# Kernel tuning notes

Measured on AMD Instinct MI355X. Metric: run time of the kernel, lower is better.

Reference implementation:

```python
import jax, jax.numpy as jnp
import numpy as np

EPS = 1e-9

def setup_inputs() -> dict:
    key = jax.random.key(0)
    ks = jax.random.split(key, 6)
    B, S, D, F, E, K = 2, 2048, 1024, 4096, 8, 2
    hidden = jax.random.normal(ks[0], (B, S, D), dtype=jnp.float32)
    expert_indices = jax.random.randint(ks[1], (B, S, K), 0, E, dtype=jnp.int32)
    expert_weights = jax.random.uniform(ks[2], (B, S, K), dtype=jnp.float32)
    # normalize like a real top-k router would
    expert_weights = expert_weights / jnp.sum(expert_weights, axis=-1, keepdims=True)
    router_logits = jax.random.normal(ks[3], (B, S, E), dtype=jnp.float32)
    w1 = jax.random.normal(ks[4], (E, D, F), dtype=jnp.float32) * (1.0 / np.sqrt(D))
    b1 = jnp.zeros((E, F), dtype=jnp.float32)
    w2 = jax.random.normal(ks[5], (E, F, D), dtype=jnp.float32) * (1.0 / np.sqrt(F))
    b2 = jnp.zeros((E, D), dtype=jnp.float32)
    return {"hidden": hidden, "expert_indices": expert_indices,
            "expert_weights": expert_weights, "router_logits": router_logits,
            "w1": w1, "b1": b1, "w2": w2, "b2": b2}

def reference(hidden, expert_indices, expert_weights, router_logits, w1, b1, w2, b2):
    # All-expert dense compute (faithful to torch.stack([expert(hidden) ...], dim=-2))
    # hidden: [B,S,D]; w1: [E,D,F]; w2: [E,F,D]
    h1 = jnp.einsum('bsd,edf->bsef', hidden, w1) + b1            # [B,S,E,F]
    h1 = jax.nn.gelu(h1)
    expert_outputs = jnp.einsum('bsef,efd->bsed', h1, w2) + b2   # [B,S,E,D]
    # gather selected experts along expert axis (torch.gather dim=-2)
    idx = expert_indices[..., None]                              # [B,S,K,1]
    selected = jnp.take_along_axis(expert_outputs, idx, axis=-2) # [B,S,K,D]
    mixed = jnp.sum(selected * expert_weights[..., None], axis=-2)  # [B,S,D]
    # observation stats
    route_probs = jax.nn.softmax(router_logits, axis=-1)
    log_p = jnp.log(jnp.clip(route_probs, EPS, None))
    route_entropy = jnp.mean(jnp.sum(-route_probs * log_p, axis=-1))
    top2 = jax.lax.top_k(route_probs, 2)[0]
    winner_margin = jnp.mean(top2[..., 0] - top2[..., -1])
    return (mixed, route_entropy, winner_margin)
```

## Files before the change

kernel.cpp:

```cpp
#include <hip/hip_runtime.h>
#include <stddef.h>
#include <stdint.h>

#define BDIM 2
#define SDIM 2048
#define DDIM 1024
#define FDIM 4096
#define ENUM 8
#define KSEL 2
#define TTOK (BDIM * SDIM)
#define PPAIR (TTOK * KSEL)
#define VOUT ((size_t)TTOK * DDIM)

typedef float f32x4 __attribute__((ext_vector_type(4)));
typedef short bf16x8 __attribute__((ext_vector_type(8)));
typedef unsigned short u16x8 __attribute__((ext_vector_type(8)));
typedef unsigned short u16x4 __attribute__((ext_vector_type(4)));

#define WAITV(N) asm volatile("s_waitcnt vmcnt(" #N ")" ::: "memory")
#define BARX() asm volatile("s_barrier" ::: "memory")

__device__ __forceinline__ unsigned short f2bf(float f) {
  unsigned int u = __float_as_uint(f);
  u += 0x7fffu + ((u >> 16) & 1u);
  return (unsigned short)(u >> 16);
}

__device__ __forceinline__ float gelu_tanh(float x) {
  float u = 0.7978845608028654f * (x + 0.044715f * x * x * x);
  float e = __expf(2.0f * u);
  float t = 1.0f - 2.0f / (e + 1.0f);
  return 0.5f * x * (1.0f + t);
}

__device__ __forceinline__ void gload16(const void* g, void* l) {
  __builtin_amdgcn_global_load_lds(
      (const __attribute__((address_space(1))) unsigned int*)g,
      (__attribute__((address_space(3))) unsigned int*)l, 16, 0, 0);
}

__global__ __launch_bounds__(256) void statsA_kernel(const float* __restrict__ lg,
                                                     float* __restrict__ pst) {
  __shared__ float se[256], sm[256];
  const int r = blockIdx.x * 256 + threadIdx.x;
  float v[ENUM];
  float mx = -1e30f;
#pragma unroll
  for (int i = 0; i < ENUM; ++i) { v[i] = lg[r * ENUM + i]; mx = fmaxf(mx, v[i]); }
  float s = 0.f;
#pragma unroll
  for (int i = 0; i < ENUM; ++i) { v[i] = __expf(v[i] - mx); s += v[i]; }
  float inv = 1.f / s;
  float p1 = -1.f, p2 = -1.f, e_ = 0.f;
#pragma unroll
  for (int i = 0; i < ENUM; ++i) {
    float p = v[i] * inv;
    e_ -= p * logf(fmaxf(p, 1e-9f));
    if (p > p1) { p2 = p1; p1 = p; } else if (p > p2) { p2 = p; }
  }
  se[threadIdx.x] = e_; sm[threadIdx.x] = p1 - p2;
  __syncthreads();
  for (int st = 128; st > 0; st >>= 1) {
    if (threadIdx.x < (unsigned)st) { se[threadIdx.x] += se[threadIdx.x + st]; sm[threadIdx.x] += sm[threadIdx.x + st]; }
    __syncthreads();
  }
  if (threadIdx.x == 0) { pst[blockIdx.x * 2] = se[0]; pst[blockIdx.x * 2 + 1] = sm[0]; }
}

__global__ void statsB_kernel(const float* __restrict__ pst, float* __restrict__ out) {
  if (threadIdx.x == 0) {
    float a = 0.f, b = 0.f;
    for (int i = 0; i < 16; ++i) { a += pst[2 * i]; b += pst[2 * i + 1]; }
    out[VOUT]     = a / (float)TTOK;
    out[VOUT + 1] = b / (float)TTOK;
  }
}

__global__ __launch_bounds__(256) void routing_kernel(const int* __restrict__ eidx,
                                                      int* __restrict__ g_cnt,
                                                      int* __restrict__ g_off,
                                                      int* __restrict__ pairTok,
                                                      int* __restrict__ inv,
                                                      int* __restrict__ b256E,
                                                      int* __restrict__ b256M,
                                                      int* __restrict__ b128E,
                                                      int* __restrict__ b128M,
                                                      int* __restrict__ nT) {
  __shared__ int sc[ENUM], so[ENUM], scur[ENUM];
  const int tid = threadIdx.x;
  if (tid < ENUM) sc[tid] = 0;
  __syncthreads();
  for (int p = tid; p < PPAIR; p += 256) atomicAdd(&sc[eidx[p]], 1);
  __syncthreads();
  if (tid == 0) {
    int o = 0, n256 = 0, n128 = 0;
    for (int e = 0; e < ENUM; ++e) {
      so[e] = o;
      const int cnt = sc[e];
      const int nf = cnt >> 8;
      const int rem = cnt - (nf << 8);
      for (int i = 0; i < nf; ++i) { b256E[n256] = e; b256M[n256] = i << 8; ++n256; }
      const int np = (rem + 127) >> 7;
      for (int j = 0; j < np; ++j) { b128E[n128] = e; b128M[n128] = (nf << 8) + (j << 7); ++n128; }
      o += cnt;
    }
    nT[0] = n256; nT[1] = n128;
  }
  __syncthreads();
  if (tid < ENUM) { scur[tid] = so[tid]; g_cnt[tid] = sc[tid]; g_off[tid] = so[tid]; }
  __syncthreads();
  for (int p = tid; p < PPAIR; p += 256) {
    int e = eidx[p];
    int pos = atomicAdd(&scur[e], 1);
    pairTok[pos] = p >> 1;
    inv[p] = pos;
  }
}

__global__ __launch_bounds__(256) void cvt_hidden_kernel(const float* __restrict__ in,
                                                         unsigned short* __restrict__ outp) {
  const int i = blockIdx.x * 256 + threadIdx.x;
  f32x4 a = ((const f32x4*)in)[(size_t)i * 2];
  f32x4 b = ((const f32x4*)in)[(size_t)i * 2 + 1];
  u16x8 o;
  o[0] = f2bf(a[0]); o[1] = f2bf(a[1]); o[2] = f2bf(a[2]); o[3] = f2bf(a[3]);
  o[4] = f2bf(b[0]); o[5] = f2bf(b[1]); o[6] = f2bf(b[2]); o[7] = f2bf(b[3]);
  ((u16x8*)outp)[i] = o;
}

__global__ __launch_bounds__(256) void transpose_cvt_kernel(const float* __restrict__ in,
                                                            unsigned short* __restrict__ outp,
                                                            int R, int C) {
  __shared__ float tile[32][33];
  const size_t base = (size_t)blockIdx.z * (size_t)R * (size_t)C;
  const float* ip = in + base;
  unsigned short* op = outp + base;
  const int r0 = blockIdx.y * 32, c0 = blockIdx.x * 32;
  const int i = threadIdx.x >> 3;
  const int j4 = (threadIdx.x & 7) << 2;
  f32x4 v = *(const f32x4*)(ip + (size_t)(r0 + i) * C + c0 + j4);
  tile[i][j4 + 0] = v[0]; tile[i][j4 + 1] = v[1]; tile[i][j4 + 2] = v[2]; tile[i][j4 + 3] = v[3];
  __syncthreads();
  u16x4 o;
  o[0] = f2bf(tile[j4 + 0][i]); o[1] = f2bf(tile[j4 + 1][i]);
  o[2] = f2bf(tile[j4 + 2][i]); o[3] = f2bf(tile[j4 + 3][i]);
  *(u16x4*)(op + (size_t)(c0 + i) * R + r0 + j4) = o;
}

__global__ __launch_bounds__(512, 2) void gemm1_kernel(const unsigned short* __restrict__ hB,
                                                       const unsigned short* __restrict__ w1T,
                                                       const float* __restrict__ b1,
                                                       const int* __restrict__ g_off,
                                                       const int* __restrict__ pairTok,
                                                       const int* __restrict__ b256E,
                                                       const int* __restrict__ b256M,
                                                       const int* __restrict__ nT,
                                                       unsigned short* __restrict__ h1) {
  const int flat = blockIdx.x + 32 * blockIdx.y;
  const int w = (flat & 7) * 64 + (flat >> 3);
  const int mI = w & 31;
  const int nB = w >> 5;
  if (mI >= nT[0]) return;
  const int e = b256E[mI];
  const int m0 = b256M[mI];
  const int off_e = g_off[e];
  const int n0 = nB << 8;

  __shared__ __align__(16) unsigned short Ah[2][2][256 * 32];
  __shared__ __align__(16) unsigned short Bh[2][2][256 * 32];

  const int tid = threadIdx.x;
  const int lane = tid & 63;
  const int wm = (tid >> 6) >> 2;
  const int wn = (tid >> 6) & 3;

  const unsigned short* gArow[2];
  const unsigned short* gBrow[2];
  int ldsOff[2];
#pragma unroll
  for (int c = 0; c < 2; ++c) {
    const int idx = c * 512 + tid;
    const int row = idx >> 2;
    const int g = (idx & 3) ^ ((row >> 1) & 3);
    ldsOff[c] = idx * 16;
    const int tok = pairTok[off_e + m0 + row];
    gArow[c] = hB + (size_t)tok * DDIM + g * 8;
    gBrow[c] = w1T + ((size_t)e * FDIM + (n0 + row)) * DDIM + g * 8;
  }

#define G1_STAGE_A(bufv, ksv, kofs) do { \
  gload16(gArow[0] + (kofs), (char*)(&Ah[(bufv)][(ksv)][0]) + ldsOff[0]); \
  gload16(gArow[1] + (kofs), (char*)(&Ah[(bufv)][(ksv)][0]) + ldsOff[1]); } while (0)
#define G1_STAGE_B(bufv, ksv, kofs) do { \
  gload16(gBrow[0] + (kofs), (char*)(&Bh[(bufv)][(ksv)][0]) + ldsOff[0]); \
  gload16(gBrow[1] + (kofs), (char*)(&Bh[(bufv)][(ksv)][0]) + ldsOff[1]); } while (0)

  const int kh = lane >> 4;
  const int l15 = lane & 15;
  int aoff[8], boff[4];
#pragma unroll
  for (int i = 0; i < 8; ++i) {
    const int r = wm * 128 + i * 16 + l15;
    aoff[i] = r * 64 + ((kh ^ ((r >> 1) & 3)) << 4);
  }
#pragma unroll
  for (int i = 0; i < 4; ++i) {
    const int r = wn * 64 + i * 16 + l15;
    boff[i] = r * 64 + ((kh ^ ((r >> 1) & 3)) << 4);
  }

  f32x4 acc[8][4];
#pragma unroll
  for (int i = 0; i < 8; ++i)
#pragma unroll
    for (int j = 0; j < 4; ++j) acc[i][j] = (f32x4){0.f, 0.f, 0.f, 0.f};

  const int KT = DDIM / 64;
  G1_STAGE_A(0, 0, 0);  G1_STAGE_B(0, 0, 0);
  G1_STAGE_A(0, 1, 32); G1_STAGE_B(0, 1, 32);
  G1_STAGE_A(1, 0, 64); G1_STAGE_B(1, 0, 64);
  G1_STAGE_A(1, 1, 96);
  WAITV(6);
  BARX();

  for (int t = 0; t < KT; ++t) {
    const int buf = t & 1;
    const int bufn = buf ^ 1;
    const int ko1 = (t + 1) * 64;
    const int ko2 = (t + 2) * 64;
    bf16x8 af[4], bv[4];
#pragma unroll
    for (int ks = 0; ks < 2; ++ks) {
#pragma unroll
      for (int i = 0; i < 4; ++i) bv[i] = *(const bf16x8*)((const char*)(&Bh[buf][ks][0]) + boff[i]);
#pragma unroll
      for (int i = 0; i < 4; ++i) af[i] = *(const bf16x8*)((const char*)(&Ah[buf][ks][0]) + aoff[i]);
      __builtin_amdgcn_s_setprio(1);
#pragma unroll
      for (int mi = 0; mi < 4; ++mi)
#pragma unroll
        for (int ni = 0; ni < 4; ++ni)
          acc[mi][ni] = __builtin_amdgcn_mfma_f32_16x16x32_bf16(af[mi], bv[ni], acc[mi][ni], 0, 0, 0);
      __builtin_amdgcn_s_setprio(0);
      if (ks == 0) { if (t + 1 < KT) G1_STAGE_B(bufn, 1, ko1 + 32); }
      else         { if (t + 2 < KT) G1_STAGE_B(buf, 0, ko2); }
      BARX();
#pragma unroll
      for (int i = 0; i < 4; ++i) af[i] = *(const bf16x8*)((const char*)(&Ah[buf][ks][0]) + aoff[4 + i]);
      __builtin_amdgcn_s_setprio(1);
#pragma unroll
      for (int mi = 0; mi < 4; ++mi)
#pragma unroll
        for (int ni = 0; ni < 4; ++ni)
          acc[4 + mi][ni] = __builtin_amdgcn_mfma_f32_16x16x32_bf16(af[mi], bv[ni], acc[4 + mi][ni], 0, 0, 0);
      __builtin_amdgcn_s_setprio(0);
      if (ks == 0) { if (t + 2 < KT) G1_STAGE_A(buf, 0, ko2); }
      else {
        if (t + 2 < KT) G1_STAGE_A(buf, 1, ko2 + 32);
        if (t < KT - 2)      { WAITV(6); }
        else if (t == KT - 2){ WAITV(0); }
      }
      BARX();
    }
  }
#undef G1_STAGE_A
#undef G1_STAGE_B

  float bias[4];
#pragma unroll
  for (int ni = 0; ni < 4; ++ni)
    bias[ni] = b1[e * FDIM + n0 + wn * 64 + ni * 16 + l15];
#pragma unroll
  for (int mi = 0; mi < 8; ++mi) {
#pragma unroll
    for (int j = 0; j < 4; ++j) {
      const int row = wm * 128 + mi * 16 + kh * 4 + j;
      unsigned short* dst = h1 + (size_t)(off_e + m0 + row) * FDIM + n0 + wn * 64;
#pragma unroll
      for (int ni = 0; ni < 4; ++ni)
        dst[ni * 16 + l15] = f2bf(gelu_tanh(acc[mi][ni][j] + bias[ni]));
    }
  }
}

__global__ __launch_bounds__(512, 2) void gemm1p_kernel(const unsigned short* __restrict__ hB,
                                                        const unsigned short* __restrict__ w1T,
                                                        const float* __restrict__ b1,
                                                        const int* __restrict__ g_cnt,
                                                        const int* __restrict__ g_off,
                                                        const int* __restrict__ pairTok,
                                                        const int* __restrict__ b128E,
                                                        const int* __restrict__ b128M,
                                                        const int* __restrict__ nT,
                                                        unsigned short* __restrict__ h1) {
  const int flat = blockIdx.x + 16 * blockIdx.y;
  const int w = (flat & 7) * 32 + (flat >> 3);
  const int mI = w & 15;
  const int nB = w >> 4;
  if (mI >= nT[1]) return;
  const int e = b128E[mI];
  const int m0 = b128M[mI];
  const int off_e = g_off[e];
  const int rows_e = min(128, g_cnt[e] - m0);
  const int n0 = nB << 8;

  __shared__ __align__(16) unsigned short As[2][128 * 64];
  __shared__ __align__(16) unsigned short Bs[2][256 * 64];

  const int tid = threadIdx.x;
  const int lane = tid & 63;
  const int wm = (tid >> 6) >> 2;
  const int wn = (tid >> 6) & 3;

  const unsigned short* gA[2];
  const unsigned short* gB[4];
  int ldsA[2], ldsB[4];
#pragma unroll
  for (int c = 0; c < 2; ++c) {
    const int p = (c * 512 + tid) * 16;
    const int row = p >> 7;
    const int g = ((p >> 4) & 7) ^ (row & 7);
    ldsA[c] = p;
    const int tok = pairTok[off_e + m0 + min(row, rows_e - 1)];
    gA[c] = hB + (size_t)tok * DDIM + (g << 3);
  }
#pragma unroll
  for (int c = 0; c < 4; ++c) {
    const int p = (c * 512 + tid) * 16;
    const int row = p >> 7;
    const int g = ((p >> 4) & 7) ^ (row & 7);
    ldsB[c] = p;
    gB[c] = w1T + ((size_t)e * FDIM + (n0 + row)) * DDIM + (g << 3);
  }

  const int kh = lane >> 4;
  const int l15 = lane & 15;
  int aoff[4][2], boff[4][2];
#pragma unroll
  for (int i = 0; i < 4; ++i) {
    const int ar = wm * 64 + i * 16 + l15;
#pragma unroll
    for (int ks = 0; ks < 2; ++ks)
      aoff[i][ks] = ar * 128 + ((((ks << 2) | kh) ^ (ar & 7)) << 4);
    const int br = wn * 64 + i * 16 + l15;
#pragma unroll
    for (int ks = 0; ks < 2; ++ks)
      boff[i][ks] = br * 128 + ((((ks << 2) | kh) ^ (br & 7)) << 4);
  }

  f32x4 acc[4][4];
#pragma unroll
  for (int i = 0; i < 4; ++i)
#pragma unroll
    for (int j = 0; j < 4; ++j) acc[i][j] = (f32x4){0.f, 0.f, 0.f, 0.f};

#pragma unroll
  for (int c = 0; c < 2; ++c) gload16(gA[c], (char*)As[0] + ldsA[c]);
#pragma unroll
  for (int c = 0; c < 4; ++c) gload16(gB[c], (char*)Bs[0] + ldsB[c]);
  WAITV(0);
  BARX();

  int cur = 0;
  const int KT = DDIM / 64;
  for (int kt = 0; kt < KT; ++kt) {
    if (kt + 1 < KT) {
#pragma unroll
      for (int c = 0; c < 2; ++c) gload16(gA[c] + (size_t)(kt + 1) * 64, (char*)As[cur ^ 1] + ldsA[c]);
#pragma unroll
      for (int c = 0; c < 4; ++c) gload16(gB[c] + (size_t)(kt + 1) * 64, (char*)Bs[cur ^ 1] + ldsB[c]);
    }
#pragma unroll
    for (int ks = 0; ks < 2; ++ks) {
      bf16x8 af[4], bv[4];
#pragma unroll
      for (int i = 0; i < 4; ++i) af[i] = *(const bf16x8*)((const char*)As[cur] + aoff[i][ks]);
#pragma unroll
      for (int i = 0; i < 4; ++i) bv[i] = *(const bf16x8*)((const char*)Bs[cur] + boff[i][ks]);
      __builtin_amdgcn_s_setprio(1);
#pragma unroll
      for (int mi = 0; mi < 4; ++mi)
#pragma unroll
        for (int ni = 0; ni < 4; ++ni)
          acc[mi][ni] = __builtin_amdgcn_mfma_f32_16x16x32_bf16(af[mi], bv[ni], acc[mi][ni], 0, 0, 0);
      __builtin_amdgcn_s_setprio(0);
    }
    WAITV(0);
    BARX();
    cur ^= 1;
  }

  float bias[4];
#pragma unroll
  for (int ni = 0; ni < 4; ++ni)
    bias[ni] = b1[e * FDIM + n0 + wn * 64 + ni * 16 + l15];
#pragma unroll
  for (int mi = 0; mi < 4; ++mi) {
#pragma unroll
    for (int j = 0; j < 4; ++j) {
      const int row = wm * 64 + mi * 16 + kh * 4 + j;
      if (row < rows_e) {
        unsigned short* dst = h1 + (size_t)(off_e + m0 + row) * FDIM + n0 + wn * 64;
#pragma unroll
        for (int ni = 0; ni < 4; ++ni)
          dst[ni * 16 + l15] = f2bf(gelu_tanh(acc[mi][ni][j] + bias[ni]));
      }
    }
  }
}

__global__ __launch_bounds__(512, 2) void gemm2_kernel(const unsigned short* __restrict__ h1,
                                                       const unsigned short* __restrict__ w2T,
                                                       const float* __restrict__ b2,
                                                       const int* __restrict__ g_off,
                                                       const int* __restrict__ b256E,
                                                       const int* __restrict__ b256M,
                                                       const int* __restrict__ nT,
                                                       float* __restrict__ h2p) {
  const int flat = blockIdx.x + 32 * blockIdx.y;
  const int w = (flat & 7) * 16 + (flat >> 3);
  const int mI = w & 31;
  const int nB = w >> 5;
  if (mI >= nT[0]) return;
  const int s = blockIdx.z;
  const int e = b256E[mI];
  const int m0 = b256M[mI];
  const int off_e = g_off[e];
  const int n0 = nB << 8;
  const int kbase = s * (FDIM / 2);

  __shared__ __align__(16) unsigned short Ah[2][2][256 * 32];
  __shared__ __align__(16) unsigned short Bh[2][2][256 * 32];

  const int tid = threadIdx.x;
  const int lane = tid & 63;
  const int wm = (tid >> 6) >> 2;
  const int wn = (tid >> 6) & 3;

  const unsigned short* gArow[2];
  const unsigned short* gBrow[2];
  int ldsOff[2];
#pragma unroll
  for (int c = 0; c < 2; ++c) {
    const int idx = c * 512 + tid;
    const int row = idx >> 2;
    const int g = (idx & 3) ^ ((row >> 1) & 3);
    ldsOff[c] = idx * 16;
    gArow[c] = h1 + (size_t)(off_e + m0 + row) * FDIM + kbase + g * 8;
    gBrow[c] = w2T + ((size_t)e * DDIM + (n0 + row)) * FDIM + kbase + g * 8;
  }

#define G2_STAGE_A(bufv, ksv, kofs) do { \
  gload16(gArow[0] + (kofs), (char*)(&Ah[(bufv)][(ksv)][0]) + ldsOff[0]); \
  gload16(gArow[1] + (kofs), (char*)(&Ah[(bufv)][(ksv)][0]) + ldsOff[1]); } while (0)
#define G2_STAGE_B(bufv, ksv, kofs) do { \
  gload16(gBrow[0] + (kofs), (char*)(&Bh[(bufv)][(ksv)][0]) + ldsOff[0]); \
  gload16(gBrow[1] + (kofs), (char*)(&Bh[(bufv)][(ksv)][0]) + ldsOff[1]); } while (0)

  const int kh = lane >> 4;
  const int l15 = lane & 15;
  int aoff[8], boff[4];
#pragma unroll
  for (int i = 0; i < 8; ++i) {
    const int r = wm * 128 + i * 16 + l15;
    aoff[i] = r * 64 + ((kh ^ ((r >> 1) & 3)) << 4);
  }
#pragma unroll
  for (int i = 0; i < 4; ++i) {
    const int r = wn * 64 + i * 16 + l15;
    boff[i] = r * 64 + ((kh ^ ((r >> 1) & 3)) << 4);
  }

  f32x4 acc[8][4];
#pragma unroll
  for (int i = 0; i < 8; ++i)
#pragma unroll
    for (int j = 0; j < 4; ++j) acc[i][j] = (f32x4){0.f, 0.f, 0.f, 0.f};

  const int KT = (FDIM / 2) / 64;
  G2_STAGE_A(0, 0, 0);  G2_STAGE_B(0, 0, 0);
  G2_STAGE_A(0, 1, 32); G2_STAGE_B(0, 1, 32);
  G2_STAGE_A(1, 0, 64); G2_STAGE_B(1, 0, 64);
  G2_STAGE_A(1, 1, 96);
  WAITV(6);
  BARX();

  for (int t = 0; t < KT; ++t) {
    const int buf = t & 1;
    const int bufn = buf ^ 1;
    const int ko1 = (t + 1) * 64;
    const int ko2 = (t + 2) * 64;
    bf16x8 af[4], bv[4];
#pragma unroll
    for (int ks = 0; ks < 2; ++ks) {
#pragma unroll
      for (int i = 0; i < 4; ++i) bv[i] = *(const bf16x8*)((const char*)(&Bh[buf][ks][0]) + boff[i]);
#pragma unroll
      for (int i = 0; i < 4; ++i) af[i] = *(const bf16x8*)((const char*)(&Ah[buf][ks][0]) + aoff[i]);
      __builtin_amdgcn_s_setprio(1);
#pragma unroll
      for (int mi = 0; mi < 4; ++mi)
#pragma unroll
        for (int ni = 0; ni < 4; ++ni)
          acc[mi][ni] = __builtin_amdgcn_mfma_f32_16x16x32_bf16(af[mi], bv[ni], acc[mi][ni], 0, 0, 0);
      __builtin_amdgcn_s_setprio(0);
      if (ks == 0) { if (t + 1 < KT) G2_STAGE_B(bufn, 1, ko1 + 32); }
      else         { if (t + 2 < KT) G2_STAGE_B(buf, 0, ko2); }
      BARX();
#pragma unroll
      for (int i = 0; i < 4; ++i) af[i] = *(const bf16x8*)((const char*)(&Ah[buf][ks][0]) + aoff[4 + i]);
      __builtin_amdgcn_s_setprio(1);
#pragma unroll
      for (int mi = 0; mi < 4; ++mi)
#pragma unroll
        for (int ni = 0; ni < 4; ++ni)
          acc[4 + mi][ni] = __builtin_amdgcn_mfma_f32_16x16x32_bf16(af[mi], bv[ni], acc[4 + mi][ni], 0, 0, 0);
      __builtin_amdgcn_s_setprio(0);
      if (ks == 0) { if (t + 2 < KT) G2_STAGE_A(buf, 0, ko2); }
      else {
        if (t + 2 < KT) G2_STAGE_A(buf, 1, ko2 + 32);
        if (t < KT - 2)      { WAITV(6); }
        else if (t == KT - 2){ WAITV(0); }
      }
      BARX();
    }
  }
#undef G2_STAGE_A
#undef G2_STAGE_B

  float* outBase = h2p + (size_t)s * PPAIR * DDIM;
#pragma unroll
  for (int mi = 0; mi < 8; ++mi) {
#pragma unroll
    for (int j = 0; j < 4; ++j) {
      const int row = wm * 128 + mi * 16 + kh * 4 + j;
      float* dp = outBase + (size_t)(off_e + m0 + row) * DDIM;
#pragma unroll
      for (int ni = 0; ni < 4; ++ni) {
        const int col = n0 + wn * 64 + ni * 16 + l15;
        float v = acc[mi][ni][j];
        if (s == 0) v += b2[e * DDIM + col];
        dp[col] = v;
      }
    }
  }
}

__global__ __launch_bounds__(512, 2) void gemm2p_kernel(const unsigned short* __restrict__ h1,
                                                        const unsigned short* __restrict__ w2T,
                                                        const float* __restrict__ b2,
                                                        const int* __restrict__ g_cnt,
                                                        const int* __restrict__ g_off,
                                                        const int* __restrict__ b128E,
                                                        const int* __restrict__ b128M,
                                                        const int* __restrict__ nT,
                                                        float* __restrict__ h2p) {
  const int flat = blockIdx.x + 16 * blockIdx.y;
  const int w = (flat & 7) * 8 + (flat >> 3);
  const int mI = w & 15;
  const int nB = w >> 4;
  if (mI >= nT[1]) return;
  const int s = blockIdx.z;
  const int e = b128E[mI];
  const int m0 = b128M[mI];
  const int off_e = g_off[e];
  const int rows_e = min(128, g_cnt[e] - m0);
  const int n0 = nB << 8;
  const int kbase = s * (FDIM / 2);

  __shared__ __align__(16) unsigned short As[2][128 * 64];
  __shared__ __align__(16) unsigned short Bs[2][256 * 64];

  const int tid = threadIdx.x;
  const int lane = tid & 63;
  const int wm = (tid >> 6) >> 2;
  const int wn = (tid >> 6) & 3;

  const unsigned short* gA[2];
  const unsigned short* gB[4];
  int ldsA[2], ldsB[4];
#pragma unroll
  for (int c = 0; c < 2; ++c) {
    const int p = (c * 512 + tid) * 16;
    const int row = p >> 7;
    const int g = ((p >> 4) & 7) ^ (row & 7);
    ldsA[c] = p;
    gA[c] = h1 + (size_t)(off_e + m0 + min(row, rows_e - 1)) * FDIM + kbase + (g << 3);
  }
#pragma unroll
  for (int c = 0; c < 4; ++c) {
    const int p = (c * 512 + tid) * 16;
    const int row = p >> 7;
    const int g = ((p >> 4) & 7) ^ (row & 7);
    ldsB[c] = p;
    gB[c] = w2T + ((size_t)e * DDIM + (n0 + row)) * FDIM + kbase + (g << 3);
  }

  const int kh = lane >> 4;
  const int l15 = lane & 15;
  int aoff[4][2], boff[4][2];
#pragma unroll
  for (int i = 0; i < 4; ++i) {
    const int ar = wm * 64 + i * 16 + l15;
    const int br = wn * 64 + i * 16 + l15;
#pragma unroll
    for (int ks = 0; ks < 2; ++ks) {
      aoff[i][ks] = ar * 128 + ((((ks << 2) | kh) ^ (ar & 7)) << 4);
      boff[i][ks] = br * 128 + ((((ks << 2) | kh) ^ (br & 7)) << 4);
    }
  }

  f32x4 acc[4][4];
#pragma unroll
  for (int i = 0; i < 4; ++i)
#pragma unroll
    for (int j = 0; j < 4; ++j) acc[i][j] = (f32x4){0.f, 0.f, 0.f, 0.f};

#pragma unroll
  for (int c = 0; c < 2; ++c) gload16(gA[c], (char*)As[0] + ldsA[c]);
#pragma unroll
  for (int c = 0; c < 4; ++c) gload16(gB[c], (char*)Bs[0] + ldsB[c]);
  WAITV(0);
  BARX();

  int cur = 0;
  const int KT = (FDIM / 2) / 64;
  for (int kt = 0; kt < KT; ++kt) {
    if (kt + 1 < KT) {
#pragma unroll
      for (int c = 0; c < 2; ++c) gload16(gA[c] + (size_t)(kt + 1) * 64, (char*)As[cur ^ 1] + ldsA[c]);
#pragma unroll
      for (int c = 0; c < 4; ++c) gload16(gB[c] + (size_t)(kt + 1) * 64, (char*)Bs[cur ^ 1] + ldsB[c]);
    }
#pragma unroll
    for (int ks = 0; ks < 2; ++ks) {
      bf16x8 af[4], bv[4];
#pragma unroll
      for (int i = 0; i < 4; ++i) af[i] = *(const bf16x8*)((const char*)As[cur] + aoff[i][ks]);
#pragma unroll
      for (int i = 0; i < 4; ++i) bv[i] = *(const bf16x8*)((const char*)Bs[cur] + boff[i][ks]);
      __builtin_amdgcn_s_setprio(1);
#pragma unroll
      for (int mi = 0; mi < 4; ++mi)
#pragma unroll
        for (int ni = 0; ni < 4; ++ni)
          acc[mi][ni] = __builtin_amdgcn_mfma_f32_16x16x32_bf16(af[mi], bv[ni], acc[mi][ni], 0, 0, 0);
      __builtin_amdgcn_s_setprio(0);
    }
    WAITV(0);
    BARX();
    cur ^= 1;
  }

  float* outBase = h2p + (size_t)s * PPAIR * DDIM;
#pragma unroll
  for (int mi = 0; mi < 4; ++mi) {
#pragma unroll
    for (int j = 0; j < 4; ++j) {
      const int row = wm * 64 + mi * 16 + kh * 4 + j;
      if (row < rows_e) {
        float* dp = outBase + (size_t)(off_e + m0 + row) * DDIM;
#pragma unroll
        for (int ni = 0; ni < 4; ++ni) {
          const int col = n0 + wn * 64 + ni * 16 + l15;
          float v = acc[mi][ni][j];
          if (s == 0) v += b2[e * DDIM + col];
          dp[col] = v;
        }
      }
    }
  }
}

__global__ __launch_bounds__(256) void combine_kernel(const float* __restrict__ h2p,
                                                      const float* __restrict__ ew,
                                                      const int* __restrict__ inv,
                                                      float* __restrict__ out) {
  const int i = blockIdx.x * 256 + threadIdx.x;
  const int t = i >> 8;
  const int c = i & 255;
  const int q0 = inv[t * 2], q1 = inv[t * 2 + 1];
  const float wa = ew[t * 2], wb = ew[t * 2 + 1];
  const f32x4* p0 = (const f32x4*)h2p;
  const f32x4* p1 = (const f32x4*)(h2p + (size_t)PPAIR * DDIM);
  f32x4 r = (p0[(size_t)q0 * 256 + c] + p1[(size_t)q0 * 256 + c]) * wa
          + (p0[(size_t)q1 * 256 + c] + p1[(size_t)q1 * 256 + c]) * wb;
  ((f32x4*)out)[i] = r;
}

extern "C" void kernel_launch(void* const* d_in, const int* in_sizes, int n_in,
                              void* d_out, int out_size, void* d_ws, size_t ws_size,
                              hipStream_t stream) {
  (void)in_sizes; (void)n_in; (void)out_size; (void)ws_size;
  const float* hidden = (const float*)d_in[0];
  const int*   eidx   = (const int*)d_in[1];
  const float* ew     = (const float*)d_in[2];
  const float* rlog   = (const float*)d_in[3];
  const float* w1     = (const float*)d_in[4];
  const float* b1     = (const float*)d_in[5];
  const float* w2     = (const float*)d_in[6];
  const float* b2     = (const float*)d_in[7];
  float* out = (float*)d_out;

  char* wsb = (char*)d_ws;
  const size_t SZ_W = (size_t)ENUM * DDIM * FDIM * 2;
  unsigned short* w1T = (unsigned short*)(wsb);
  unsigned short* w2T = (unsigned short*)(wsb + SZ_W);
  unsigned short* hB  = (unsigned short*)(wsb + 2 * SZ_W);
  unsigned short* h1  = (unsigned short*)(wsb + 2 * SZ_W + (size_t)TTOK * DDIM * 2);
  int* g_cnt   = (int*)(wsb + 2 * SZ_W + (size_t)TTOK * DDIM * 2 + (size_t)PPAIR * FDIM * 2);
  int* g_off   = g_cnt + 8;
  int* pairTok = g_off + 8;
  int* inv     = pairTok + PPAIR;
  int* b256E   = inv + PPAIR;
  int* b256M   = b256E + 32;
  int* b128E   = b256M + 32;
  int* b128M   = b128E + 16;
  int* nT      = b128M + 16;
  float* pstats = (float*)(nT + 2);
  float* h2p = (float*)wsb;

  statsA_kernel<<<16, 256, 0, stream>>>(rlog, pstats);
  statsB_kernel<<<1, 64, 0, stream>>>(pstats, out);
  routing_kernel<<<1, 256, 0, stream>>>(eidx, g_cnt, g_off, pairTok, inv, b256E, b256M, b128E, b128M, nT);
  cvt_hidden_kernel<<<(TTOK * DDIM / 8 + 255) / 256, 256, 0, stream>>>(hidden, hB);
  transpose_cvt_kernel<<<dim3(FDIM / 32, DDIM / 32, ENUM), 256, 0, stream>>>(w1, w1T, DDIM, FDIM);
  transpose_cvt_kernel<<<dim3(DDIM / 32, FDIM / 32, ENUM), 256, 0, stream>>>(w2, w2T, FDIM, DDIM);
  gemm1_kernel<<<dim3(32, 16), 512, 0, stream>>>(hB, w1T, b1, g_off, pairTok, b256E, b256M, nT, h1);
  gemm1p_kernel<<<dim3(16, 16), 512, 0, stream>>>(hB, w1T, b1, g_cnt, g_off, pairTok, b128E, b128M, nT, h1);
  gemm2_kernel<<<dim3(32, 4, 2), 512, 0, stream>>>(h1, w2T, b2, g_off, b256E, b256M, nT, h2p);
  gemm2p_kernel<<<dim3(16, 4, 2), 512, 0, stream>>>(h1, w2T, b2, g_cnt, g_off, b128E, b128M, nT, h2p);
  combine_kernel<<<(TTOK * DDIM / 4) / 256, 256, 0, stream>>>(h2p, ew, inv, out);
}
```

Measured before the change: 385.5 us.

## Merge preprocessing, transposes and full/partial GEMM tile kernels into fewer launches

Folds hidden conversion, router stats and routing into one multi-role pre_kernel, and both weight transposes into a single launch. The full-tile and partial-tile GEMM kernels for each stage are merged into one grid that branches on tile index over a shared LDS pool, so full and partial tiles share one wave. The aim is fewer kernel launches and less tail idle time between dependent kernels. The risk is that the single routing block now runs alongside the conversion blocks, and the merged GEMMs use a larger shared-memory footprint that could limit occupancy for the partial-tile path.

```diff
diff --git a/kernel.cpp b/kernel.cpp
--- a/kernel.cpp
+++ b/kernel.cpp
@@ -39,55 +39,60 @@
       (__attribute__((address_space(3))) unsigned int*)l, 16, 0, 0);
 }
 
-__global__ __launch_bounds__(256) void statsA_kernel(const float* __restrict__ lg,
-                                                     float* __restrict__ pst) {
-  __shared__ float se[256], sm[256];
-  const int r = blockIdx.x * 256 + threadIdx.x;
-  float v[ENUM];
-  float mx = -1e30f;
-#pragma unroll
-  for (int i = 0; i < ENUM; ++i) { v[i] = lg[r * ENUM + i]; mx = fmaxf(mx, v[i]); }
-  float s = 0.f;
-#pragma unroll
-  for (int i = 0; i < ENUM; ++i) { v[i] = __expf(v[i] - mx); s += v[i]; }
-  float inv = 1.f / s;
-  float p1 = -1.f, p2 = -1.f, e_ = 0.f;
-#pragma unroll
-  for (int i = 0; i < ENUM; ++i) {
-    float p = v[i] * inv;
-    e_ -= p * logf(fmaxf(p, 1e-9f));
-    if (p > p1) { p2 = p1; p1 = p; } else if (p > p2) { p2 = p; }
-  }
-  se[threadIdx.x] = e_; sm[threadIdx.x] = p1 - p2;
-  __syncthreads();
-  for (int st = 128; st > 0; st >>= 1) {
-    if (threadIdx.x < (unsigned)st) { se[threadIdx.x] += se[threadIdx.x + st]; sm[threadIdx.x] += sm[threadIdx.x + st]; }
+__global__ __launch_bounds__(256) void pre_kernel(const float* __restrict__ hidden,
+                                                  unsigned short* __restrict__ hB,
+                                                  const float* __restrict__ lg,
+                                                  float* __restrict__ pst,
+                                                  const int* __restrict__ eidx,
+                                                  int* __restrict__ g_cnt,
+                                                  int* __restrict__ g_off,
+                                                  int* __restrict__ pairTok,
+                                                  int* __restrict__ inv,
+                                                  int* __restrict__ b256E,
+                                                  int* __restrict__ b256M,
+                                                  int* __restrict__ b128E,
+                                                  int* __restrict__ b128M,
+                                                  int* __restrict__ nT) {
+  const int b = blockIdx.x;
+  const int tid = threadIdx.x;
+  if (b < 2048) {
+    const int i = b * 256 + tid;
+    f32x4 a = ((const f32x4*)hidden)[(size_t)i * 2];
+    f32x4 c = ((const f32x4*)hidden)[(size_t)i * 2 + 1];
+    u16x8 o;
+    o[0] = f2bf(a[0]); o[1] = f2bf(a[1]); o[2] = f2bf(a[2]); o[3] = f2bf(a[3]);
+    o[4] = f2bf(c[0]); o[5] = f2bf(c[1]); o[6] = f2bf(c[2]); o[7] = f2bf(c[3]);
+    ((u16x8*)hB)[i] = o;
+    return;
+  }
+  if (b < 2064) {
+    __shared__ float se[256], sm[256];
+    const int r = (b - 2048) * 256 + tid;
+    float v[ENUM];
+    float mx = -1e30f;
+#pragma unroll
+    for (int i = 0; i < ENUM; ++i) { v[i] = lg[r * ENUM + i]; mx = fmaxf(mx, v[i]); }
+    float s = 0.f;
+#pragma unroll
+    for (int i = 0; i < ENUM; ++i) { v[i] = __expf(v[i] - mx); s += v[i]; }
+    float invs = 1.f / s;
+    float p1 = -1.f, p2 = -1.f, e_ = 0.f;
+#pragma unroll
+    for (int i = 0; i < ENUM; ++i) {
+      float p = v[i] * invs;
+      e_ -= p * logf(fmaxf(p, 1e-9f));
+      if (p > p1) { p2 = p1; p1 = p; } else if (p > p2) { p2 = p; }
+    }
+    se[tid] = e_; sm[tid] = p1 - p2;
     __syncthreads();
-  }
-  if (threadIdx.x == 0) { pst[blockIdx.x * 2] = se[0]; pst[blockIdx.x * 2 + 1] = sm[0]; }
-}
-
-__global__ void statsB_kernel(const float* __restrict__ pst, float* __restrict__ out) {
-  if (threadIdx.x == 0) {
-    float a = 0.f, b = 0.f;
-    for (int i = 0; i < 16; ++i) { a += pst[2 * i]; b += pst[2 * i + 1]; }
-    out[VOUT]     = a / (float)TTOK;
-    out[VOUT + 1] = b / (float)TTOK;
-  }
-}
-
-__global__ __launch_bounds__(256) void routing_kernel(const int* __restrict__ eidx,
-                                                      int* __restrict__ g_cnt,
-                                                      int* __restrict__ g_off,
-                                                      int* __restrict__ pairTok,
-                                                      int* __restrict__ inv,
-                                                      int* __restrict__ b256E,
-                                                      int* __restrict__ b256M,
-                                                      int* __restrict__ b128E,
-                                                      int* __restrict__ b128M,
-                                                      int* __restrict__ nT) {
+    for (int st = 128; st > 0; st >>= 1) {
+      if (tid < (unsigned)st) { se[tid] += se[tid + st]; sm[tid] += sm[tid + st]; }
+      __syncthreads();
+    }
+    if (tid == 0) { pst[(b - 2048) * 2] = se[0]; pst[(b - 2048) * 2 + 1] = sm[0]; }
+    return;
+  }
   __shared__ int sc[ENUM], so[ENUM], scur[ENUM];
-  const int tid = threadIdx.x;
   if (tid < ENUM) sc[tid] = 0;
   __syncthreads();
   for (int p = tid; p < PPAIR; p += 256) atomicAdd(&sc[eidx[p]], 1);
@@ -117,25 +122,33 @@
   }
 }
 
-__global__ __launch_bounds__(256) void cvt_hidden_kernel(const float* __restrict__ in,
-                                                         unsigned short* __restrict__ outp) {
-  const int i = blockIdx.x * 256 + threadIdx.x;
-  f32x4 a = ((const f32x4*)in)[(size_t)i * 2];
-  f32x4 b = ((const f32x4*)in)[(size_t)i * 2 + 1];
-  u16x8 o;
-  o[0] = f2bf(a[0]); o[1] = f2bf(a[1]); o[2] = f2bf(a[2]); o[3] = f2bf(a[3]);
-  o[4] = f2bf(b[0]); o[5] = f2bf(b[1]); o[6] = f2bf(b[2]); o[7] = f2bf(b[3]);
-  ((u16x8*)outp)[i] = o;
-}
-
-__global__ __launch_bounds__(256) void transpose_cvt_kernel(const float* __restrict__ in,
-                                                            unsigned short* __restrict__ outp,
-                                                            int R, int C) {
+__global__ void statsB_kernel(const float* __restrict__ pst, float* __restrict__ out) {
+  if (threadIdx.x == 0) {
+    float a = 0.f, b = 0.f;
+    for (int i = 0; i < 16; ++i) { a += pst[2 * i]; b += pst[2 * i + 1]; }
+    out[VOUT]     = a / (float)TTOK;
+    out[VOUT + 1] = b / (float)TTOK;
+  }
+}
+
+__global__ __launch_bounds__(256) void transpose2_kernel(const float* __restrict__ w1,
+                                                         unsigned short* __restrict__ w1T,
+                                                         const float* __restrict__ w2,
+                                                         unsigned short* __restrict__ w2T) {
   __shared__ float tile[32][33];
-  const size_t base = (size_t)blockIdx.z * (size_t)R * (size_t)C;
-  const float* ip = in + base;
-  unsigned short* op = outp + base;
-  const int r0 = blockIdx.y * 32, c0 = blockIdx.x * 32;
+  const int z = blockIdx.y;
+  const int b = blockIdx.x;
+  const float* ip; unsigned short* op; int C, r0, c0;
+  if (z < 8) {
+    const size_t base = (size_t)z * DDIM * FDIM;
+    ip = w1 + base; op = w1T + base; C = FDIM;
+    c0 = (b & 127) << 5; r0 = (b >> 7) << 5;
+  } else {
+    const size_t base = (size_t)(z - 8) * DDIM * FDIM;
+    ip = w2 + base; op = w2T + base; C = DDIM;
+    c0 = (b & 31) << 5; r0 = (b >> 5) << 5;
+  }
+  const int R = (z < 8) ? DDIM : FDIM;
   const int i = threadIdx.x >> 3;
   const int j4 = (threadIdx.x & 7) << 2;
   f32x4 v = *(const f32x4*)(ip + (size_t)(r0 + i) * C + c0 + j4);
@@ -147,518 +160,391 @@
   *(u16x4*)(op + (size_t)(c0 + i) * R + r0 + j4) = o;
 }
 
-__global__ __launch_bounds__(512, 2) void gemm1_kernel(const unsigned short* __restrict__ hB,
-                                                       const unsigned short* __restrict__ w1T,
-                                                       const float* __restrict__ b1,
-                                                       const int* __restrict__ g_off,
-                                                       const int* __restrict__ pairTok,
-                                                       const int* __restrict__ b256E,
-                                                       const int* __restrict__ b256M,
-                                                       const int* __restrict__ nT,
-                                                       unsigned short* __restrict__ h1) {
-  const int flat = blockIdx.x + 32 * blockIdx.y;
-  const int w = (flat & 7) * 64 + (flat >> 3);
-  const int mI = w & 31;
-  const int nB = w >> 5;
-  if (mI >= nT[0]) return;
-  const int e = b256E[mI];
-  const int m0 = b256M[mI];
-  const int off_e = g_off[e];
+__global__ __launch_bounds__(512, 2) void gemm1_fused(const unsigned short* __restrict__ hB,
+                                                      const unsigned short* __restrict__ w1T,
+                                                      const float* __restrict__ b1,
+                                                      const int* __restrict__ g_cnt,
+                                                      const int* __restrict__ g_off,
+                                                      const int* __restrict__ pairTok,
+                                                      const int* __restrict__ b256E,
+                                                      const int* __restrict__ b256M,
+                                                      const int* __restrict__ b128E,
+                                                      const int* __restrict__ b128M,
+                                                      const int* __restrict__ nT,
+                                                      unsigned short* __restrict__ h1) {
+  __shared__ __align__(16) char smem[131072];
+  const int flat = blockIdx.x + 48 * blockIdx.y;
+  const int w = (flat & 7) * 96 + (flat >> 3);
+  const int mIdx = w % 48;
+  const int nB = w / 48;
   const int n0 = nB << 8;
-
-  __shared__ __align__(16) unsigned short Ah[2][2][256 * 32];
-  __shared__ __align__(16) unsigned short Bh[2][2][256 * 32];
 
   const int tid = threadIdx.x;
   const int lane = tid & 63;
   const int wm = (tid >> 6) >> 2;
   const int wn = (tid >> 6) & 3;
-
-  const unsigned short* gArow[2];
-  const unsigned short* gBrow[2];
-  int ldsOff[2];
-#pragma unroll
-  for (int c = 0; c < 2; ++c) {
-    const int idx = c * 512 + tid;
-    const int row = idx >> 2;
-    const int g = (idx & 3) ^ ((row >> 1) & 3);
-    ldsOff[c] = idx * 16;
-    const int tok = pairTok[off_e + m0 + row];
-    gArow[c] = hB + (size_t)tok * DDIM + g * 8;
-    gBrow[c] = w1T + ((size_t)e * FDIM + (n0 + row)) * DDIM + g * 8;
-  }
-
-#define G1_STAGE_A(bufv, ksv, kofs) do { \
-  gload16(gArow[0] + (kofs), (char*)(&Ah[(bufv)][(ksv)][0]) + ldsOff[0]); \
-  gload16(gArow[1] + (kofs), (char*)(&Ah[(bufv)][(ksv)][0]) + ldsOff[1]); } while (0)
-#define G1_STAGE_B(bufv, ksv, kofs) do { \
-  gload16(gBrow[0] + (kofs), (char*)(&Bh[(bufv)][(ksv)][0]) + ldsOff[0]); \
-  gload16(gBrow[1] + (kofs), (char*)(&Bh[(bufv)][(ksv)][0]) + ldsOff[1]); } while (0)
-
   const int kh = lane >> 4;
   const int l15 = lane & 15;
-  int aoff[8], boff[4];
-#pragma unroll
-  for (int i = 0; i < 8; ++i) {
-    const int r = wm * 128 + i * 16 + l15;
-    aoff[i] = r * 64 + ((kh ^ ((r >> 1) & 3)) << 4);
-  }
-#pragma unroll
-  for (int i = 0; i < 4; ++i) {
-    const int r = wn * 64 + i * 16 + l15;
-    boff[i] = r * 64 + ((kh ^ ((r >> 1) & 3)) << 4);
-  }
-
-  f32x4 acc[8][4];
-#pragma unroll
-  for (int i = 0; i < 8; ++i)
-#pragma unroll
-    for (int j = 0; j < 4; ++j) acc[i][j] = (f32x4){0.f, 0.f, 0.f, 0.f};
-
-  const int KT = DDIM / 64;
-  G1_STAGE_A(0, 0, 0);  G1_STAGE_B(0, 0, 0);
-  G1_STAGE_A(0, 1, 32); G1_STAGE_B(0, 1, 32);
-  G1_STAGE_A(1, 0, 64); G1_STAGE_B(1, 0, 64);
-  G1_STAGE_A(1, 1, 96);
-  WAITV(6);
-  BARX();
-
-  for (int t = 0; t < KT; ++t) {
-    const int buf = t & 1;
-    const int bufn = buf ^ 1;
-    const int ko1 = (t + 1) * 64;
-    const int ko2 = (t + 2) * 64;
-    bf16x8 af[4], bv[4];
-#pragma unroll
-    for (int ks = 0; ks < 2; ++ks) {
-#pragma unroll
-      for (int i = 0; i < 4; ++i) bv[i] = *(const bf16x8*)((const char*)(&Bh[buf][ks][0]) + boff[i]);
-#pragma unroll
-      for (int i = 0; i < 4; ++i) af[i] = *(const bf16x8*)((const char*)(&Ah[buf][ks][0]) + aoff[i]);
-      __builtin_amdgcn_s_setprio(1);
-#pragma unroll
-      for (int mi = 0; mi < 4; ++mi)
-#pragma unroll
-        for (int ni = 0; ni < 4; ++ni)
-          acc[mi][ni] = __builtin_amdgcn_mfma_f32_16x16x32_bf16(af[mi], bv[ni], acc[mi][ni], 0, 0, 0);
-      __builtin_amdgcn_s_setprio(0);
-      if (ks == 0) { if (t + 1 < KT) G1_STAGE_B(bufn, 1, ko1 + 32); }
-      else         { if (t + 2 < KT) G1_STAGE_B(buf, 0, ko2); }
-      BARX();
-#pragma unroll
-      for (int i = 0; i < 4; ++i) af[i] = *(const bf16x8*)((const char*)(&Ah[buf][ks][0]) + aoff[4 + i]);
-      __builtin_amdgcn_s_setprio(1);
-#pragma unroll
-      for (int mi = 0; mi < 4; ++mi)
-#pragma unroll
-        for (int ni = 0; ni < 4; ++ni)
-          acc[4 + mi][ni] = __builtin_amdgcn_mfma_f32_16x16x32_bf16(af[mi], bv[ni], acc[4 + mi][ni], 0, 0, 0);
-      __builtin_amdgcn_s_setprio(0);
-      if (ks == 0) { if (t + 2 < KT) G1_STAGE_A(buf, 0, ko2); }
-      else {
-        if (t + 2 < KT) G1_STAGE_A(buf, 1, ko2 + 32);
-        if (t < KT - 2)      { WAITV(6); }
-        else if (t == KT - 2){ WAITV(0); }
-      }
-      BARX();
-    }
-  }
+
+  if (mIdx < 32) {
+    if (mIdx >= nT[0]) return;
+    const int e = b256E[mIdx];
+    const int m0 = b256M[mIdx];
+    const int off_e = g_off[e];
+
+    const unsigned short* gArow[2];
+    const unsigned short* gBrow[2];
+    int ldsOff[2];
+#pragma unroll
+    for (int c = 0; c < 2; ++c) {
+      const int idx = c * 512 + tid;
+      const int row = idx >> 2;
+      const int g = (idx & 3) ^ ((row >> 1) & 3);
+      ldsOff[c] = idx * 16;
+      const int tok = pairTok[off_e + m0 + row];
+      gArow[c] = hB + (size_t)tok * DDIM + g * 8;
+      gBrow[c] = w1T + ((size_t)e * FDIM + (n0 + row)) * DDIM + g * 8;
+    }
+
+#define AH_OFF(bufv, ksv) (((bufv) * 2 + (ksv)) * 16384)
+#define BH_OFF(bufv, ksv) (65536 + ((bufv) * 2 + (ksv)) * 16384)
+#define G1_STAGE_A(bufv, ksv, kofs) do { \
+    gload16(gArow[0] + (kofs), smem + AH_OFF(bufv, ksv) + ldsOff[0]); \
+    gload16(gArow[1] + (kofs), smem + AH_OFF(bufv, ksv) + ldsOff[1]); } while (0)
+#define G1_STAGE_B(bufv, ksv, kofs) do { \
+    gload16(gBrow[0] + (kofs), smem + BH_OFF(bufv, ksv) + ldsOff[0]); \
+    gload16(gBrow[1] + (kofs), smem + BH_OFF(bufv, ksv) + ldsOff[1]); } while (0)
+
+    int aoff[8], boff[4];
+#pragma unroll
+    for (int i = 0; i < 8; ++i) {
+      const int r = wm * 128 + i * 16 + l15;
+      aoff[i] = r * 64 + ((kh ^ ((r >> 1) & 3)) << 4);
+    }
+#pragma unroll
+    for (int i = 0; i < 4; ++i) {
+      const int r = wn * 64 + i * 16 + l15;
+      boff[i] = r * 64 + ((kh ^ ((r >> 1) & 3)) << 4);
+    }
+
+    f32x4 acc[8][4];
+#pragma unroll
+    for (int i = 0; i < 8; ++i)
+#pragma unroll
+      for (int j = 0; j < 4; ++j) acc[i][j] = (f32x4){0.f, 0.f, 0.f, 0.f};
+
+    const int KT = DDIM / 64;
+    G1_STAGE_A(0, 0, 0);  G1_STAGE_B(0, 0, 0);
+    G1_STAGE_A(0, 1, 32); G1_STAGE_B(0, 1, 32);
+    G1_STAGE_A(1, 0, 64); G1_STAGE_B(1, 0, 64);
+    G1_STAGE_A(1, 1, 96);
+    WAITV(6);
+    BARX();
+
+    for (int t = 0; t < KT; ++t) {
+      const int buf = t & 1;
+      const int bufn = buf ^ 1;
+      const int ko1 = (t + 1) * 64;
+      const int ko2 = (t + 2) * 64;
+      bf16x8 af[4], bv[4];
+#pragma unroll
+      for (int ks = 0; ks < 2; ++ks) {
+#pragma unroll
+        for (int i = 0; i < 4; ++i) bv[i] = *(const bf16x8*)(smem + BH_OFF(buf, ks) + boff[i]);
+#pragma unroll
+        for (int i = 0; i < 4; ++i) af[i] = *(const bf16x8*)(smem + AH_OFF(buf, ks) + aoff[i]);
+        __builtin_amdgcn_s_setprio(1);
+#pragma unroll
+        for (int mi = 0; mi < 4; ++mi)
+#pragma unroll
+          for (int ni = 0; ni < 4; ++ni)
+            acc[mi][ni] = __builtin_amdgcn_mfma_f32_16x16x32_bf16(af[mi], bv[ni], acc[mi][ni], 0, 0, 0);
+        __builtin_amdgcn_s_setprio(0);
+        if (ks == 0) { if (t + 1 < KT) G1_STAGE_B(bufn, 1, ko1 + 32); }
+        else         { if (t + 2 < KT) G1_STAGE_B(buf, 0, ko2); }
+        BARX();
+#pragma unroll
+        for (int i = 0; i < 4; ++i) af[i] = *(const bf16x8*)(smem + AH_OFF(buf, ks) + aoff[4 + i]);
+        __builtin_amdgcn_s_setprio(1);
+#pragma unroll
+        for (int mi = 0; mi < 4; ++mi)
+#pragma unroll
+          for (int ni = 0; ni < 4; ++ni)
+            acc[4 + mi][ni] = __builtin_amdgcn_mfma_f32_16x16x32_bf16(af[mi], bv[ni], acc[4 + mi][ni], 0, 0, 0);
+        __builtin_amdgcn_s_setprio(0);
+        if (ks == 0) { if (t + 2 < KT) G1_STAGE_A(buf, 0, ko2); }
+        else {
+          if (t + 2 < KT) G1_STAGE_A(buf, 1, ko2 + 32);
+          if (t < KT - 2)      { WAITV(6); }
+          else if (t == KT - 2){ WAITV(0); }
+        }
+        BARX();
+      }
+    }
 #undef G1_STAGE_A
 #undef G1_STAGE_B
-
-  float bias[4];
-#pragma unroll
-  for (int ni = 0; ni < 4; ++ni)
-    bias[ni] = b1[e * FDIM + n0 + wn * 64 + ni * 16 + l15];
-#pragma unroll
-  for (int mi = 0; mi < 8; ++mi) {
-#pragma unroll
-    for (int j = 0; j < 4; ++j) {
-      const int row = wm * 128 + mi * 16 + kh * 4 + j;
-      unsigned short* dst = h1 + (size_t)(off_e + m0 + row) * FDIM + n0 + wn * 64;
-#pragma unroll
-      for (int ni = 0; ni < 4; ++ni)
-        dst[ni * 16 + l15] = f2bf(gelu_tanh(acc[mi][ni][j] + bias[ni]));
-    }
-  }
-}
-
-__global__ __launch_bounds__(512, 2) void gemm1p_kernel(const unsigned short* __restrict__ hB,
-                                                        const unsigned short* __restrict__ w1T,
-                                                        const float* __restrict__ b1,
-                                                        const int* __restrict__ g_cnt,
-                                                        const int* __restrict__ g_off,
-                                                        const int* __restrict__ pairTok,
-                                                        const int* __restrict__ b128E,
-                                                        const int* __restrict__ b128M,
-                                                        const int* __restrict__ nT,
-                                                        unsigned short* __restrict__ h1) {
-  const int flat = blockIdx.x + 16 * blockIdx.y;
-  const int w = (flat & 7) * 32 + (flat >> 3);
-  const int mI = w & 15;
-  const int nB = w >> 4;
-  if (mI >= nT[1]) return;
-  const int e = b128E[mI];
-  const int m0 = b128M[mI];
-  const int off_e = g_off[e];
-  const int rows_e = min(128, g_cnt[e] - m0);
+#undef AH_OFF
+#undef BH_OFF
+
+    float bias[4];
+#pragma unroll
+    for (int ni = 0; ni < 4; ++ni)
+      bias[ni] = b1[e * FDIM + n0 + wn * 64 + ni * 16 + l15];
+#pragma unroll
+    for (int mi = 0; mi < 8; ++mi) {
+#pragma unroll
+      for (int j = 0; j < 4; ++j) {
+        const int row = wm * 128 + mi * 16 + kh * 4 + j;
+        unsigned short* dst = h1 + (size_t)(off_e + m0 + row) * FDIM + n0 + wn * 64;
+#pragma unroll
+        for (int ni = 0; ni < 4; ++ni)
+          dst[ni * 16 + l15] = f2bf(gelu_tanh(acc[mi][ni][j] + bias[ni]));
+      }
+    }
+    return;
+  }
+
+  {
+    const int mI = mIdx - 32;
+    if (mI >= nT[1]) return;
+    const int e = b128E[mI];
+    const int m0 = b128M[mI];
+    const int off_e = g_off[e];
+    const int rows_e = min(128, g_cnt[e] - m0);
+
+    unsigned short* As = (unsigned short*)smem;
+    unsigned short* Bs = (unsigned short*)(smem + 32768);
+    const int ABUF = 128 * 64;
+    const int BBUF = 256 * 64;
+
+    const unsigned short* gA[2];
+    const unsigned short* gB[4];
+    int ldsA[2], ldsB[4];
+#pragma unroll
+    for (int c = 0; c < 2; ++c) {
+      const int p = (c * 512 + tid) * 16;
+      const int row = p >> 7;
+      const int g = ((p >> 4) & 7) ^ (row & 7);
+      ldsA[c] = p;
+      const int tok = pairTok[off_e + m0 + min(row, rows_e - 1)];
+      gA[c] = hB + (size_t)tok * DDIM + (g << 3);
+    }
+#pragma unroll
+    for (int c = 0; c < 4; ++c) {
+      const int p = (c * 512 + tid) * 16;
+      const int row = p >> 7;
+      const int g = ((p >> 4) & 7) ^ (row & 7);
+      ldsB[c] = p;
+      gB[c] = w1T + ((size_t)e * FDIM + (n0 + row)) * DDIM + (g << 3);
+    }
+
+    int aoff[4][2], boff[4][2];
+#pragma unroll
+    for (int i = 0; i < 4; ++i) {
+      const int ar = wm * 64 + i * 16 + l15;
+      const int br = wn * 64 + i * 16 + l15;
+#pragma unroll
+      for (int ks = 0; ks < 2; ++ks) {
+        aoff[i][ks] = ar * 128 + ((((ks << 2) | kh) ^ (ar & 7)) << 4);
+        boff[i][ks] = br * 128 + ((((ks << 2) | kh) ^ (br & 7)) << 4);
+      }
+    }
+
+    f32x4 acc[4][4];
+#pragma unroll
+    for (int i = 0; i < 4; ++i)
+#pragma unroll
+      for (int j = 0; j < 4; ++j) acc[i][j] = (f32x4){0.f, 0.f, 0.f, 0.f};
+
+#pragma unroll
+    for (int c = 0; c < 2; ++c) gload16(gA[c], (char*)As + ldsA[c]);
+#pragma unroll
+    for (int c = 0; c < 4; ++c) gload16(gB[c], (char*)Bs + ldsB[c]);
+    WAITV(0);
+    BARX();
+
+    int cur = 0;
+    const int KT = DDIM / 64;
+    for (int kt = 0; kt < KT; ++kt) {
+      if (kt + 1 < KT) {
+#pragma unroll
+        for (int c = 0; c < 2; ++c) gload16(gA[c] + (size_t)(kt + 1) * 64, (char*)(As + (cur ^ 1) * ABUF) + ldsA[c]);
+#pragma unroll
+        for (int c = 0; c < 4; ++c) gload16(gB[c] + (size_t)(kt + 1) * 64, (char*)(Bs + (cur ^ 1) * BBUF) + ldsB[c]);
+      }
+#pragma unroll
+      for (int ks = 0; ks < 2; ++ks) {
+        bf16x8 af[4], bv[4];
+#pragma unroll
+        for (int i = 0; i < 4; ++i) af[i] = *(const bf16x8*)((const char*)(As + cur * ABUF) + aoff[i][ks]);
+#pragma unroll
+        for (int i = 0; i < 4; ++i) bv[i] = *(const bf16x8*)((const char*)(Bs + cur * BBUF) + boff[i][ks]);
+        __builtin_amdgcn_s_setprio(1);
+#pragma unroll
+        for (int mi = 0; mi < 4; ++mi)
+#pragma unroll
+          for (int ni = 0; ni < 4; ++ni)
+            acc[mi][ni] = __builtin_amdgcn_mfma_f32_16x16x32_bf16(af[mi], bv[ni], acc[mi][ni], 0, 0, 0);
+        __builtin_amdgcn_s_setprio(0);
+      }
+      WAITV(0);
+      BARX();
+      cur ^= 1;
+    }
+
+    float bias[4];
+#pragma unroll
+    for (int ni = 0; ni < 4; ++ni)
+      bias[ni] = b1[e * FDIM + n0 + wn * 64 + ni * 16 + l15];
+#pragma unroll
+    for (int mi = 0; mi < 4; ++mi) {
+#pragma unroll
+      for (int j = 0; j < 4; ++j) {
+        const int row = wm * 64 + mi * 16 + kh * 4 + j;
+        if (row < rows_e) {
+          unsigned short* dst = h1 + (size_t)(off_e + m0 + row) * FDIM + n0 + wn * 64;
+#pragma unroll
+          for (int ni = 0; ni < 4; ++ni)
+            dst[ni * 16 + l15] = f2bf(gelu_tanh(acc[mi][ni][j] + bias[ni]));
+        }
+      }
+    }
+  }
+}
+
+__global__ __launch_bounds__(512, 2) void gemm2_fused(const unsigned short* __restrict__ h1,
+                                                      const unsigned short* __restrict__ w2T,
+                                                      const float* __restrict__ b2,
+                                                      const int* __restrict__ g_cnt,
+                                                      const int* __restrict__ g_off,
+                                                      const int* __restrict__ b256E,
+                                                      const int* __restrict__ b256M,
+                                                      const int* __restrict__ b128E,
+                                                      const int* __restrict__ b128M,
+                                                      const int* __restrict__ nT,
+                                                      float* __restrict__ h2p) {
+  __shared__ __align__(16) char smem[131072];
+  const int flat = blockIdx.x + 48 * blockIdx.y + 192 * blockIdx.z;
+  const int w = (flat & 7) * 48 + (flat >> 3);
+  const int mIdx = w % 48;
+  const int rest = w / 48;
+  const int nB = rest & 3;
+  const int s = rest >> 2;
   const int n0 = nB << 8;
-
-  __shared__ __align__(16) unsigned short As[2][128 * 64];
-  __shared__ __align__(16) unsigned short Bs[2][256 * 64];
+  const int kbase = s * (FDIM / 2);
 
   const int tid = threadIdx.x;
   const int lane = tid & 63;
   const int wm = (tid >> 6) >> 2;
   const int wn = (tid >> 6) & 3;
-
-  const unsigned short* gA[2];
-  const unsigned short* gB[4];
-  int ldsA[2], ldsB[4];
-#pragma unroll
-  for (int c = 0; c < 2; ++c) {
-    const int p = (c * 512 + tid) * 16;
-    const int row = p >> 7;
-    const int g = ((p >> 4) & 7) ^ (row & 7);
-    ldsA[c] = p;
-    const int tok = pairTok[off_e + m0 + min(row, rows_e - 1)];
-    gA[c] = hB + (size_t)tok * DDIM + (g << 3);
-  }
-#pragma unroll
-  for (int c = 0; c < 4; ++c) {
-    const int p = (c * 512 + tid) * 16;
-    const int row = p >> 7;
-    const int g = ((p >> 4) & 7) ^ (row & 7);
-    ldsB[c] = p;
-    gB[c] = w1T + ((size_t)e * FDIM + (n0 + row)) * DDIM + (g << 3);
-  }
-
   const int kh = lane >> 4;
   const int l15 = lane & 15;
-  int aoff[4][2], boff[4][2];
-#pragma unroll
-  for (int i = 0; i < 4; ++i) {
-    const int ar = wm * 64 + i * 16 + l15;
-#pragma unroll
-    for (int ks = 0; ks < 2; ++ks)
-      aoff[i][ks] = ar * 128 + ((((ks << 2) | kh) ^ (ar & 7)) << 4);
-    const int br = wn * 64 + i * 16 + l15;
-#pragma unroll
-    for (int ks = 0; ks < 2; ++ks)
-      boff[i][ks] = br * 128 + ((((ks << 2) | kh) ^ (br & 7)) << 4);
-  }
-
-  f32x4 acc[4][4];
-#pragma unroll
-  for (int i = 0; i < 4; ++i)
-#pragma unroll
-    for (int j = 0; j < 4; ++j) acc[i][j] = (f32x4){0.f, 0.f, 0.f, 0.f};
-
-#pragma unroll
-  for (int c = 0; c < 2; ++c) gload16(gA[c], (char*)As[0] + ldsA[c]);
-#pragma unroll
-  for (int c = 0; c < 4; ++c) gload16(gB[c], (char*)Bs[0] + ldsB[c]);
-  WAITV(0);
-  BARX();
-
-  int cur = 0;
-  const int KT = DDIM / 64;
-  for (int kt = 0; kt < KT; ++kt) {
-    if (kt + 1 < KT) {
-#pragma unroll
-      for (int c = 0; c < 2; ++c) gload16(gA[c] + (size_t)(kt + 1) * 64, (char*)As[cur ^ 1] + ldsA[c]);
-#pragma unroll
-      for (int c = 0; c < 4; ++c) gload16(gB[c] + (size_t)(kt + 1) * 64, (char*)Bs[cur ^ 1] + ldsB[c]);
-    }
-#pragma unroll
-    for (int ks = 0; ks < 2; ++ks) {
+
+  if (mIdx < 32) {
+    if (mIdx >= nT[0]) return;
+    const int e = b256E[mIdx];
+    const int m0 = b256M[mIdx];
+    const int off_e = g_off[e];
+
+    const unsigned short* gArow[2];
+    const unsigned short* gBrow[2];
+    int ldsOff[2];
+#pragma unroll
+    for (int c = 0; c < 2; ++c) {
+      const int idx = c * 512 + tid;
+      const int row = idx >> 2;
+      const int g = (idx & 3) ^ ((row >> 1) & 3);
+      ldsOff[c] = idx * 16;
+      gArow[c] = h1 + (size_t)(off_e + m0 + row) * FDIM + kbase + g * 8;
+      gBrow[c] = w2T + ((size_t)e * DDIM + (n0 + row)) * FDIM + kbase + g * 8;
+    }
+
+#define AH_OFF(bufv, ksv) (((bufv) * 2 + (ksv)) * 16384)
+#define BH_OFF(bufv, ksv) (65536 + ((bufv) * 2 + (ksv)) * 16384)
+#define G2_STAGE_A(bufv, ksv, kofs) do { \
+    gload16(gArow[0] + (kofs), smem + AH_OFF(bufv, ksv) + ldsOff[0]); \
+    gload16(gArow[1] + (kofs), smem + AH_OFF(bufv, ksv) + ldsOff[1]); } while (0)
+#define G2_STAGE_B(bufv, ksv, kofs) do { \
+    gload16(gBrow[0] + (kofs), smem + BH_OFF(bufv, ksv) + ldsOff[0]); \
+    gload16(gBrow[1] + (kofs), smem + BH_OFF(bufv, ksv) + ldsOff[1]); } while (0)
+
+    int aoff[8], boff[4];
+#pragma unroll
+    for (int i = 0; i < 8; ++i) {
+      const int r = wm * 128 + i * 16 + l15;
+      aoff[i] = r * 64 + ((kh ^ ((r >> 1) & 3)) << 4);
+    }
+#pragma unroll
+    for (int i = 0; i < 4; ++i) {
+      const int r = wn * 64 + i * 16 + l15;
+      boff[i] = r * 64 + ((kh ^ ((r >> 1) & 3)) << 4);
+    }
+
+    f32x4 acc[8][4];
+#pragma unroll
+    for (int i = 0; i < 8; ++i)
+#pragma unroll
+      for (int j = 0; j < 4; ++j) acc[i][j] = (f32x4){0.f, 0.f, 0.f, 0.f};
+
+    const int KT = (FDIM / 2) / 64;
+    G2_STAGE_A(0, 0, 0);  G2_STAGE_B(0, 0, 0);
+    G2_STAGE_A(0, 1, 32); G2_STAGE_B(0, 1, 32);
+    G2_STAGE_A(1, 0, 64); G2_STAGE_B(1, 0, 64);
+    G2_STAGE_A(1, 1, 96);
+    WAITV(6);
+    BARX();
+
+    for (int t = 0; t < KT; ++t) {
+      const int buf = t & 1;
+      const int bufn = buf ^ 1;
+      const int ko1 = (t + 1) * 64;
+      const int ko2 = (t + 2) * 64;
       bf16x8 af[4], bv[4];
 #pragma unroll
-      for (int i = 0; i < 4; ++i) af[i] = *(const bf16x8*)((const char*)As[cur] + aoff[i][ks]);
-#pragma unroll
-      for (int i = 0; i < 4; ++i) bv[i] = *(const bf16x8*)((const char*)Bs[cur] + boff[i][ks]);
-      __builtin_amdgcn_s_setprio(1);
-#pragma unroll
-      for (int mi = 0; mi < 4; ++mi)
-#pragma unroll
-        for (int ni = 0; ni < 4; ++ni)
-          acc[mi][ni] = __builtin_amdgcn_mfma_f32_16x16x32_bf16(af[mi], bv[ni], acc[mi][ni], 0, 0, 0);
-      __builtin_amdgcn_s_setprio(0);
-    }
-    WAITV(0);
-    BARX();
-    cur ^= 1;
-  }
-
-  float bias[4];
-#pragma unroll
-  for (int ni = 0; ni < 4; ++ni)
-    bias[ni] = b1[e * FDIM + n0 + wn * 64 + ni * 16 + l15];
-#pragma unroll
-  for (int mi = 0; mi < 4; ++mi) {
-#pragma unroll
-    for (int j = 0; j < 4; ++j) {
-      const int row = wm * 64 + mi * 16 + kh * 4 + j;
-      if (row < rows_e) {
-        unsigned short* dst = h1 + (size_t)(off_e + m0 + row) * FDIM + n0 + wn * 64;
-#pragma unroll
-        for (int ni = 0; ni < 4; ++ni)
-          dst[ni * 16 + l15] = f2bf(gelu_tanh(acc[mi][ni][j] + bias[ni]));
-      }
-    }
-  }
-}
-
-__global__ __launch_bounds__(512, 2) void gemm2_kernel(const unsigned short* __restrict__ h1,
-                                                       const unsigned short* __restrict__ w2T,
-                                                       const float* __restrict__ b2,
-                                                       const int* __restrict__ g_off,
-                                                       const int* __restrict__ b256E,
-                                                       const int* __restrict__ b256M,
-                                                       const int* __restrict__ nT,
-                                                       float* __restrict__ h2p) {
-  const int flat = blockIdx.x + 32 * blockIdx.y;
-  const int w = (flat & 7) * 16 + (flat >> 3);
-  const int mI = w & 31;
-  const int nB = w >> 5;
-  if (mI >= nT[0]) return;
-  const int s = blockIdx.z;
-  const int e = b256E[mI];
-  const int m0 = b256M[mI];
-  const int off_e = g_off[e];
-  const int n0 = nB << 8;
-  const int kbase = s * (FDIM / 2);
-
-  __shared__ __align__(16) unsigned short Ah[2][2][256 * 32];
-  __shared__ __align__(16) unsigned short Bh[2][2][256 * 32];
-
-  const int tid = threadIdx.x;
-  const int lane = tid & 63;
-  const int wm = (tid >> 6) >> 2;
-  const int wn = (tid >> 6) & 3;
-
-  const unsigned short* gArow[2];
-  const unsigned short* gBrow[2];
-  int ldsOff[2];
-#pragma unroll
-  for (int c = 0; c < 2; ++c) {
-    const int idx = c * 512 + tid;
-    const int row = idx >> 2;
-    const int g = (idx & 3) ^ ((row >> 1) & 3);
-    ldsOff[c] = idx * 16;
-    gArow[c] = h1 + (size_t)(off_e + m0 + row) * FDIM + kbase + g * 8;
-    gBrow[c] = w2T + ((size_t)e * DDIM + (n0 + row)) * FDIM + kbase + g * 8;
-  }
-
-#define G2_STAGE_A(bufv, ksv, kofs) do { \
-  gload16(gArow[0] + (kofs), (char*)(&Ah[(bufv)][(ksv)][0]) + ldsOff[0]); \
-  gload16(gArow[1] + (kofs), (char*)(&Ah[(bufv)][(ksv)][0]) + ldsOff[1]); } while (0)
-#define G2_STAGE_B(bufv, ksv, kofs) do { \
-  gload16(gBrow[0] + (kofs), (char*)(&Bh[(bufv)][(ksv)][0]) + ldsOff[0]); \
-  gload16(gBrow[1] + (kofs), (char*)(&Bh[(bufv)][(ksv)][0]) + ldsOff[1]); } while (0)
-
-  const int kh = lane >> 4;
-  const int l15 = lane & 15;
-  int aoff[8], boff[4];
-#pragma unroll
-  for (int i = 0; i < 8; ++i) {
-    const int r = wm * 128 + i * 16 + l15;
-    aoff[i] = r * 64 + ((kh ^ ((r >> 1) & 3)) << 4);
-  }
-#pragma unroll
-  for (int i = 0; i < 4; ++i) {
-    const int r = wn * 64 + i * 16 + l15;
-    boff[i] = r * 64 + ((kh ^ ((r >> 1) & 3)) << 4);
-  }
-
-  f32x4 acc[8][4];
-#pragma unroll
-  for (int i = 0; i < 8; ++i)
-#pragma unroll
-    for (int j = 0; j < 4; ++j) acc[i][j] = (f32x4){0.f, 0.f, 0.f, 0.f};
-
-  const int KT = (FDIM / 2) / 64;
-  G2_STAGE_A(0, 0, 0);  G2_STAGE_B(0, 0, 0);
-  G2_STAGE_A(0, 1, 32); G2_STAGE_B(0, 1, 32);
-  G2_STAGE_A(1, 0, 64); G2_STAGE_B(1, 0, 64);
-  G2_STAGE_A(1, 1, 96);
-  WAITV(6);
-  BARX();
-
-  for (int t = 0; t < KT; ++t) {
-    const int buf = t & 1;
-    const int bufn = buf ^ 1;
-    const int ko1 = (t + 1) * 64;
-    const int ko2 = (t + 2) * 64;
-    bf16x8 af[4], bv[4];
-#pragma unroll
-    for (int ks = 0; ks < 2; ++ks) {
-#pragma unroll
-      for (int i = 0; i < 4; ++i) bv[i] = *(const bf16x8*)((const char*)(&Bh[buf][ks][0]) + boff[i]);
-#pragma unroll
-      for (int i = 0; i < 4; ++i) af[i] = *(const bf16x8*)((const char*)(&Ah[buf][ks][0]) + aoff[i]);
-      __builtin_amdgcn_s_setprio(1);
-#pragma unroll
-      for (int mi = 0; mi < 4; ++mi)
-#pragma unroll
-        for (int ni = 0; ni < 4; ++ni)
-          acc[mi][ni] = __builtin_amdgcn_mfma_f32_16x16x32_bf16(af[mi], bv[ni], acc[mi][ni], 0, 0, 0);
-      __builtin_amdgcn_s_setprio(0);
-      if (ks == 0) { if (t + 1 < KT) G2_STAGE_B(bufn, 1, ko1 + 32); }
-      else         { if (t + 2 < KT) G2_STAGE_B(buf, 0, ko2); }
-      BARX();
-#pragma unroll
-      for (int i = 0; i < 4; ++i) af[i] = *(const bf16x8*)((const char*)(&Ah[buf][ks][0]) + aoff[4 + i]);
-      __builtin_amdgcn_s_setprio(1);
-#pragma unroll
-      for (int mi = 0; mi < 4; ++mi)
-#pragma unroll
-        for (int ni = 0; ni < 4; ++ni)
-          acc[4 + mi][ni] = __builtin_amdgcn_mfma_f32_16x16x32_bf16(af[mi], bv[ni], acc[4 + mi][ni], 0, 0, 0);
-      __builtin_amdgcn_s_setprio(0);
-      if (ks == 0) { if (t + 2 < KT) G2_STAGE_A(buf, 0, ko2); }
-      else {
-        if (t + 2 < KT) G2_STAGE_A(buf, 1, ko2 + 32);
-        if (t < KT - 2)      { WAITV(6); }
-        else if (t == KT - 2){ WAITV(0); }
-      }
-      BARX();
-    }
-  }
+      for (int ks = 0; ks < 2; ++ks) {
+#pragma unroll
+        for (int i = 0; i < 4; ++i) bv[i] = *(const bf16x8*)(smem + BH_OFF(buf, ks) + boff[i]);
+#pragma unroll
+        for (int i = 0; i < 4; ++i) af[i] = *(const bf16x8*)(smem + AH_OFF(buf, ks) + aoff[i]);
+        __builtin_amdgcn_s_setprio(1);
+#pragma unroll
+        for (int mi = 0; mi < 4; ++mi)
+#pragma unroll
+          for (int ni = 0; ni < 4; ++ni)
+            acc[mi][ni] = __builtin_amdgcn_mfma_f32_16x16x32_bf16(af[mi], bv[ni], acc[mi][ni], 0, 0, 0);
+        __builtin_amdgcn_s_setprio(0);
+        if (ks == 0) { if (t + 1 < KT) G2_STAGE_B(bufn, 1, ko1 + 32); }
+        else         { if (t + 2 < KT) G2_STAGE_B(buf, 0, ko2); }
+        BARX();
+#pragma unroll
+        for (int i = 0; i < 4; ++i) af[i] = *(const bf16x8*)(smem + AH_OFF(buf, ks) + aoff[4 + i]);
+        __builtin_amdgcn_s_setprio(1);
+#pragma unroll
+        for (int mi = 0; mi < 4; ++mi)
+#pragma unroll
+          for (int ni = 0; ni < 4; ++ni)
+            acc[4 + mi][ni] = __builtin_amdgcn_mfma_f32_16x16x32_bf16(af[mi], bv[ni], acc[4 + mi][ni], 0, 0, 0);
+        __builtin_amdgcn_s_setprio(0);
+        if (ks == 0) { if (t + 2 < KT) G2_STAGE_A(buf, 0, ko2); }
+        else {
+          if (t + 2 < KT) G2_STAGE_A(buf, 1, ko2 + 32);
+          if (t < KT - 2)      { WAITV(6); }
+          else if (t == KT - 2){ WAITV(0); }
+        }
+        BARX();
+      }
+    }
 #undef G2_STAGE_A
 #undef G2_STAGE_B
-
-  float* outBase = h2p + (size_t)s * PPAIR * DDIM;
-#pragma unroll
-  for (int mi = 0; mi < 8; ++mi) {
-#pragma unroll
-    for (int j = 0; j < 4; ++j) {
-      const int row = wm * 128 + mi * 16 + kh * 4 + j;
-      float* dp = outBase + (size_t)(off_e + m0 + row) * DDIM;
-#pragma unroll
-      for (int ni = 0; ni < 4; ++ni) {
-        const int col = n0 + wn * 64 + ni * 16 + l15;
-        float v = acc[mi][ni][j];
-        if (s == 0) v += b2[e * DDIM + col];
-        dp[col] = v;
-      }
-    }
-  }
-}
-
-__global__ __launch_bounds__(512, 2) void gemm2p_kernel(const unsigned short* __restrict__ h1,
-                                                        const unsigned short* __restrict__ w2T,
-                                                        const float* __restrict__ b2,
-                                                        const int* __restrict__ g_cnt,
-                                                        const int* __restrict__ g_off,
-                                                        const int* __restrict__ b128E,
-                                                        const int* __restrict__ b128M,
-                                                        const int* __restrict__ nT,
-                                                        float* __restrict__ h2p) {
-  const int flat = blockIdx.x + 16 * blockIdx.y;
-  const int w = (flat & 7) * 8 + (flat >> 3);
-  const int mI = w & 15;
-  const int nB = w >> 4;
-  if (mI >= nT[1]) return;
-  const int s = blockIdx.z;
-  const int e = b128E[mI];
-  const int m0 = b128M[mI];
-  const int off_e = g_off[e];
-  const int rows_e = min(128, g_cnt[e] - m0);
-  const int n0 = nB << 8;
-  const int kbase = s * (FDIM / 2);
-
-  __shared__ __align__(16) unsigned short As[2][128 * 64];
-  __shared__ __align__(16) unsigned short Bs[2][256 * 64];
-
-  const int tid = threadIdx.x;
-  const int lane = tid & 63;
-  const int wm = (tid >> 6) >> 2;
-  const int wn = (tid >> 6) & 3;
-
-  const unsigned short* gA[2];
-  const unsigned short* gB[4];
-  int ldsA[2], ldsB[4];
-#pragma unroll
-  for (int c = 0; c < 2; ++c) {
-    const int p = (c * 512 + tid) * 16;
-    const int row = p >> 7;
-    const int g = ((p >> 4) & 7) ^ (row & 7);
-    ldsA[c] = p;
-    gA[c] = h1 + (size_t)(off_e + m0 + min(row, rows_e - 1)) * FDIM + kbase + (g << 3);
-  }
-#pragma unroll
-  for (int c = 0; c < 4; ++c) {
-    const int p = (c * 512 + tid) * 16;
-    const int row = p >> 7;
-    const int g = ((p >> 4) & 7) ^ (row & 7);
-    ldsB[c] = p;
-    gB[c] = w2T + ((size_t)e * DDIM + (n0 + row)) * FDIM + kbase + (g << 3);
-  }
-
-  const int kh = lane >> 4;
-  const int l15 = lane & 15;
-  int aoff[4][2], boff[4][2];
-#pragma unroll
-  for (int i = 0; i < 4; ++i) {
-    const int ar = wm * 64 + i * 16 + l15;
-    const int br = wn * 64 + i * 16 + l15;
-#pragma unroll
-    for (int ks = 0; ks < 2; ++ks) {
-      aoff[i][ks] = ar * 128 + ((((ks << 2) | kh) ^ (ar & 7)) << 4);
-      boff[i][ks] = br * 128 + ((((ks << 2) | kh) ^ (br & 7)) << 4);
-    }
-  }
-
-  f32x4 acc[4][4];
-#pragma unroll
-  for (int i = 0; i < 4; ++i)
-#pragma unroll
-    for (int j = 0; j < 4; ++j) acc[i][j] = (f32x4){0.f, 0.f, 0.f, 0.f};
-
-#pragma unroll
-  for (int c = 0; c < 2; ++c) gload16(gA[c], (char*)As[0] + ldsA[c]);
-#pragma unroll
-  for (int c = 0; c < 4; ++c) gload16(gB[c], (char*)Bs[0] + ldsB[c]);
-  WAITV(0);
-  BARX();
-
-  int cur = 0;
-  const int KT = (FDIM / 2) / 64;
-  for (int kt = 0; kt < KT; ++kt) {
-    if (kt + 1 < KT) {
-#pragma unroll
-      for (int c = 0; c < 2; ++c) gload16(gA[c] + (size_t)(kt + 1) * 64, (char*)As[cur ^ 1] + ldsA[c]);
-#pragma unroll
-      for (int c = 0; c < 4; ++c) gload16(gB[c] + (size_t)(kt + 1) * 64, (char*)Bs[cur ^ 1] + ldsB[c]);
-    }
-#pragma unroll
-    for (int ks = 0; ks < 2; ++ks) {
-      bf16x8 af[4], bv[4];
-#pragma unroll
-      for (int i = 0; i < 4; ++i) af[i] = *(const bf16x8*)((const char*)As[cur] + aoff[i][ks]);
-#pragma unroll
-      for (int i = 0; i < 4; ++i) bv[i] = *(const bf16x8*)((const char*)Bs[cur] + boff[i][ks]);
-      __builtin_amdgcn_s_setprio(1);
-#pragma unroll
-      for (int mi = 0; mi < 4; ++mi)
-#pragma unroll
-        for (int ni = 0; ni < 4; ++ni)
-          acc[mi][ni] = __builtin_amdgcn_mfma_f32_16x16x32_bf16(af[mi], bv[ni], acc[mi][ni], 0, 0, 0);
-      __builtin_amdgcn_s_setprio(0);
-    }
-    WAITV(0);
-    BARX();
-    cur ^= 1;
-  }
-
-  float* outBase = h2p + (size_t)s * PPAIR * DDIM;
-#pragma unroll
-  for (int mi = 0; mi < 4; ++mi) {
-#pragma unroll
-    for (int j = 0; j < 4; ++j) {
-      const int row = wm * 64 + mi * 16 + kh * 4 + j;
-      if (row < rows_e) {
+#undef AH_OFF
+#undef BH_OFF
+
+    float* outBase = h2p + (size_t)s * PPAIR * DDIM;
+#pragma unroll
+    for (int mi = 0; mi < 8; ++mi) {
+#pragma unroll
+      for (int j = 0; j < 4; ++j) {
+        const int row = wm * 128 + mi * 16 + kh * 4 + j;
         float* dp = outBase + (size_t)(off_e + m0 + row) * DDIM;
 #pragma unroll
         for (int ni = 0; ni < 4; ++ni) {
@@ -666,6 +552,114 @@
           float v = acc[mi][ni][j];
           if (s == 0) v += b2[e * DDIM + col];
           dp[col] = v;
+        }
+      }
+    }
+    return;
+  }
+
+  {
+    const int mI = mIdx - 32;
+    if (mI >= nT[1]) return;
+    const int e = b128E[mI];
+    const int m0 = b128M[mI];
+    const int off_e = g_off[e];
+    const int rows_e = min(128, g_cnt[e] - m0);
+
+    unsigned short* As = (unsigned short*)smem;
+    unsigned short* Bs = (unsigned short*)(smem + 32768);
+    const int ABUF = 128 * 64;
+    const int BBUF = 256 * 64;
+
+    const unsigned short* gA[2];
+    const unsigned short* gB[4];
+    int ldsA[2], ldsB[4];
+#pragma unroll
+    for (int c = 0; c < 2; ++c) {
+      const int p = (c * 512 + tid) * 16;
+      const int row = p >> 7;
+      const int g = ((p >> 4) & 7) ^ (row & 7);
+      ldsA[c] = p;
+      gA[c] = h1 + (size_t)(off_e + m0 + min(row, rows_e - 1)) * FDIM + kbase + (g << 3);
+    }
+#pragma unroll
+    for (int c = 0; c < 4; ++c) {
+      const int p = (c * 512 + tid) * 16;
+      const int row = p >> 7;
+      const int g = ((p >> 4) & 7) ^ (row & 7);
+      ldsB[c] = p;
+      gB[c] = w2T + ((size_t)e * DDIM + (n0 + row)) * FDIM + kbase + (g << 3);
+    }
+
+    int aoff[4][2], boff[4][2];
+#pragma unroll
+    for (int i = 0; i < 4; ++i) {
+      const int ar = wm * 64 + i * 16 + l15;
+      const int br = wn * 64 + i * 16 + l15;
+#pragma unroll
+      for (int ks = 0; ks < 2; ++ks) {
+        aoff[i][ks] = ar * 128 + ((((ks << 2) | kh) ^ (ar & 7)) << 4);
+        boff[i][ks] = br * 128 + ((((ks << 2) | kh) ^ (br & 7)) << 4);
+      }
+    }
+
+    f32x4 acc[4][4];
+#pragma unroll
+    for (int i = 0; i < 4; ++i)
+#pragma unroll
+      for (int j = 0; j < 4; ++j) acc[i][j] = (f32x4){0.f, 0.f, 0.f, 0.f};
+
+#pragma unroll
+    for (int c = 0; c < 2; ++c) gload16(gA[c], (char*)As + ldsA[c]);
+#pragma unroll
+    for (int c = 0; c < 4; ++c) gload16(gB[c], (char*)Bs + ldsB[c]);
+    WAITV(0);
+    BARX();
+
+    int cur = 0;
+    const int KT = (FDIM / 2) / 64;
+    for (int kt = 0; kt < KT; ++kt) {
+      if (kt + 1 < KT) {
+#pragma unroll
+        for (int c = 0; c < 2; ++c) gload16(gA[c] + (size_t)(kt + 1) * 64, (char*)(As + (cur ^ 1) * ABUF) + ldsA[c]);
+#pragma unroll
+        for (int c = 0; c < 4; ++c) gload16(gB[c] + (size_t)(kt + 1) * 64, (char*)(Bs + (cur ^ 1) * BBUF) + ldsB[c]);
+      }
+#pragma unroll
+      for (int ks = 0; ks < 2; ++ks) {
+        bf16x8 af[4], bv[4];
+#pragma unroll
+        for (int i = 0; i < 4; ++i) af[i] = *(const bf16x8*)((const char*)(As + cur * ABUF) + aoff[i][ks]);
+#pragma unroll
+        for (int i = 0; i < 4; ++i) bv[i] = *(const bf16x8*)((const char*)(Bs + cur * BBUF) + boff[i][ks]);
+        __builtin_amdgcn_s_setprio(1);
+#pragma unroll
+        for (int mi = 0; mi < 4; ++mi)
+#pragma unroll
+          for (int ni = 0; ni < 4; ++ni)
+            acc[mi][ni] = __builtin_amdgcn_mfma_f32_16x16x32_bf16(af[mi], bv[ni], acc[mi][ni], 0, 0, 0);
+        __builtin_amdgcn_s_setprio(0);
+      }
+      WAITV(0);
+      BARX();
+      cur ^= 1;
+    }
+
+    float* outBase = h2p + (size_t)s * PPAIR * DDIM;
+#pragma unroll
+    for (int mi = 0; mi < 4; ++mi) {
+#pragma unroll
+      for (int j = 0; j < 4; ++j) {
+        const int row = wm * 64 + mi * 16 + kh * 4 + j;
+        if (row < rows_e) {
+          float* dp = outBase + (size_t)(off_e + m0 + row) * DDIM;
+#pragma unroll
+          for (int ni = 0; ni < 4; ++ni) {
+            const int col = n0 + wn * 64 + ni * 16 + l15;
+            float v = acc[mi][ni][j];
+            if (s == 0) v += b2[e * DDIM + col];
+            dp[col] = v;
+          }
         }
       }
     }
@@ -720,15 +714,13 @@
   float* pstats = (float*)(nT + 2);
   float* h2p = (float*)wsb;
 
-  statsA_kernel<<<16, 256, 0, stream>>>(rlog, pstats);
+  pre_kernel<<<2065, 256, 0, stream>>>(hidden, hB, rlog, pstats, eidx, g_cnt, g_off,
+                                       pairTok, inv, b256E, b256M, b128E, b128M, nT);
   statsB_kernel<<<1, 64, 0, stream>>>(pstats, out);
-  routing_kernel<<<1, 256, 0, stream>>>(eidx, g_cnt, g_off, pairTok, inv, b256E, b256M, b128E, b128M, nT);
-  cvt_hidden_kernel<<<(TTOK * DDIM / 8 + 255) / 256, 256, 0, stream>>>(hidden, hB);
-  transpose_cvt_kernel<<<dim3(FDIM / 32, DDIM / 32, ENUM), 256, 0, stream>>>(w1, w1T, DDIM, FDIM);
-  transpose_cvt_kernel<<<dim3(DDIM / 32, FDIM / 32, ENUM), 256, 0, stream>>>(w2, w2T, FDIM, DDIM);
-  gemm1_kernel<<<dim3(32, 16), 512, 0, stream>>>(hB, w1T, b1, g_off, pairTok, b256E, b256M, nT, h1);
-  gemm1p_kernel<<<dim3(16, 16), 512, 0, stream>>>(hB, w1T, b1, g_cnt, g_off, pairTok, b128E, b128M, nT, h1);
-  gemm2_kernel<<<dim3(32, 4, 2), 512, 0, stream>>>(h1, w2T, b2, g_off, b256E, b256M, nT, h2p);
-  gemm2p_kernel<<<dim3(16, 4, 2), 512, 0, stream>>>(h1, w2T, b2, g_cnt, g_off, b128E, b128M, nT, h2p);
+  transpose2_kernel<<<dim3(4096, 16), 256, 0, stream>>>(w1, w1T, w2, w2T);
+  gemm1_fused<<<dim3(48, 16), 512, 0, stream>>>(hB, w1T, b1, g_cnt, g_off, pairTok,
+                                                b256E, b256M, b128E, b128M, nT, h1);
+  gemm2_fused<<<dim3(48, 4, 2), 512, 0, stream>>>(h1, w2T, b2, g_cnt, g_off,
+                                                  b256E, b256M, b128E, b128M, nT, h2p);
   combine_kernel<<<(TTOK * DDIM / 4) / 256, 256, 0, stream>>>(h2p, ew, inv, out);
 }
```

Result: faster. 323.5 us (-16.1%).
